# Performance work log

Measured on AMD Instinct MI355X. Metric: run time of the kernel, lower is better.

Reference implementation:

```python
import jax, jax.numpy as jnp
import numpy as np

B, S, EMBED = 8, 2048, 512
FFN = 2048
N_QUBITS = 10
DEPTH = 2


def _apply_1q(state, mats, wire):
    # state: (N,) + (2,)*n complex; mats: (N,2,2) per-token or (2,2) shared
    s = jnp.moveaxis(state, 1 + wire, 1)
    shp = s.shape
    s = s.reshape(shp[0], 2, -1)
    if mats.ndim == 3:
        s = jnp.einsum('nab,nbr->nar', mats, s)
    else:
        s = jnp.einsum('ab,nbr->nar', mats, s)
    return jnp.moveaxis(s.reshape(shp), 1, 1 + wire)


def _cnot(state, ctrl, tgt):
    # CNOT: flip target axis on the control=1 slice
    ca, ta = 1 + ctrl, 1 + tgt
    s0 = jax.lax.index_in_dim(state, 0, axis=ca, keepdims=True)
    s1 = jax.lax.index_in_dim(state, 1, axis=ca, keepdims=True)
    s1 = jnp.flip(s1, axis=ta)
    return jnp.concatenate([s0, s1], axis=ca)


def _qlayer(x_flat, theta, n_qubits=N_QUBITS, depth=DEPTH):
    # x_flat: (N, n_qubits) RX encoding angles; theta: (n_qubits,) RY params
    N = x_flat.shape[0]
    state = jnp.zeros((N,) + (2,) * n_qubits, jnp.complex64)
    state = state.at[(slice(None),) + (0,) * n_qubits].set(1.0)
    # encoder: RX(x_i) on wire i, per-token angles
    for w in range(n_qubits):
        a = x_flat[:, w] * 0.5
        c = jnp.cos(a).astype(jnp.complex64)
        s = (-1j * jnp.sin(a)).astype(jnp.complex64)
        mats = jnp.stack([jnp.stack([c, s], -1), jnp.stack([s, c], -1)], -2)  # (N,2,2)
        state = _apply_1q(state, mats, w)
    # trainable RY(theta_w) on each wire (shared across tokens)
    for w in range(n_qubits):
        a = theta[w] * 0.5
        c, s = jnp.cos(a), jnp.sin(a)
        mat = jnp.stack([jnp.stack([c, -s]), jnp.stack([s, c])]).astype(jnp.complex64)
        state = _apply_1q(state, mat, w)
    # depth rounds of ring CNOT chain
    for _ in range(depth):
        for w in range(n_qubits - 1):
            state = _cnot(state, w, w + 1)
        state = _cnot(state, n_qubits - 1, 0)
    # MeasureAll PauliZ: <Z_w> per wire
    probs = jnp.abs(state.reshape(N, -1)) ** 2  # (N, 2^n)
    bits = (jnp.arange(2 ** n_qubits)[None, :] >> (n_qubits - 1 - jnp.arange(n_qubits))[:, None]) & 1
    z = (1 - 2 * bits).astype(probs.dtype)  # (n, 2^n)
    return probs @ z.T  # (N, n)


def setup_inputs() -> dict:
    key = jax.random.key(0)
    k = jax.random.split(key, 6)
    x = jax.random.normal(k[0], (B, S, EMBED), jnp.float32)
    ry_theta = jax.random.uniform(k[1], (N_QUBITS,), jnp.float32, 0.0, 2.0 * np.pi)
    W1 = jax.random.normal(k[2], (FFN, N_QUBITS), jnp.float32) / np.sqrt(N_QUBITS)
    b1 = jax.random.normal(k[3], (FFN,), jnp.float32) * 0.01
    W2 = jax.random.normal(k[4], (EMBED, FFN), jnp.float32) / np.sqrt(FFN)
    b2 = jax.random.normal(k[5], (EMBED,), jnp.float32) * 0.01
    return {"x": x, "ry_theta": ry_theta, "W1": W1, "b1": b1, "W2": W2, "b2": b2}


def reference(x, ry_theta, W1, b1, W2, b2):
    b, s, _ = x.shape
    xf = x.reshape(b * s, -1)[:, :N_QUBITS]  # encoder only uses first n_qubits feats
    q = _qlayer(xf, ry_theta).reshape(b, s, N_QUBITS)
    # dropout is identity at eval; linear1 -> relu -> linear2
    h = jax.nn.relu(q @ W1.T + b1)
    return h @ W2.T + b2
```

## Files before the change

### kernel.cpp

```cpp
#include <hip/hip_runtime.h>
#include <hip/hip_bf16.h>


typedef __attribute__((ext_vector_type(8))) short bf16x8;
typedef __attribute__((ext_vector_type(16))) float f32x16;
typedef __attribute__((ext_vector_type(8))) unsigned short us8;
typedef unsigned int u32;

#define NTOK  16384
#define EMBED 512
#define FFN   2048
#define NQ    10
#define BM    128
#define BN    128

__device__ __forceinline__ unsigned short f2bf(float f) {
  union { float f; unsigned int u; } a; a.f = f;
  unsigned int r = a.u + 0x7FFFu + ((a.u >> 16) & 1u);
  return (unsigned short)(r >> 16);
}

__device__ __forceinline__ void gload_lds16(const void* g, void* l) {
  __builtin_amdgcn_global_load_lds(
      (const __attribute__((address_space(1))) unsigned int*)g,
      (__attribute__((address_space(3))) unsigned int*)l, 16, 0, 0);
}

__global__ __launch_bounds__(256) void k_cvt_w2(const float* __restrict__ W2,
                                                unsigned short* __restrict__ W2b) {
  int gid = blockIdx.x * 256 + threadIdx.x;
  int idx = gid * 8;
  int row = idx >> 11;
  int c   = (idx >> 3) & 255;
  int pair = c >> 4, cl = c & 15;
  int slot = cl ^ (row & 15);
  float4 v0 = *(const float4*)(W2 + idx);
  float4 v1 = *(const float4*)(W2 + idx + 4);
  us8 o;
  o[0] = f2bf(v0.x); o[1] = f2bf(v0.y); o[2] = f2bf(v0.z); o[3] = f2bf(v0.w);
  o[4] = f2bf(v1.x); o[5] = f2bf(v1.y); o[6] = f2bf(v1.z); o[7] = f2bf(v1.w);
  *(us8*)(W2b + (size_t)row * FFN + pair * 128 + slot * 8) = o;
}

__global__ __launch_bounds__(256) void k_cvt_w1f(const float* __restrict__ W1,
                                                 const float* __restrict__ b1,
                                                 unsigned short* __restrict__ W1f) {
  int gid = blockIdx.x * 256 + threadIdx.x;
  int l = gid & 63, blk = gid >> 6;
  int k = blk * 32 + (l & 31);
  int wg = (l >> 5) * 8;
  us8 o;
#pragma unroll
  for (int e = 0; e < 8; ++e) {
    int wire = wg + e;
    float v = (wire < NQ) ? W1[k * NQ + wire] : (wire == NQ ? b1[k] : 0.f);
    o[e] = f2bf(v);
  }
  *(us8*)(W1f + (size_t)gid * 8) = o;
}

__global__ __launch_bounds__(256) void k_q(const float* __restrict__ x,
                                           const float* __restrict__ theta,
                                           unsigned short* __restrict__ Qf) {
  int gid = blockIdx.x * 256 + threadIdx.x;
  int l = gid & 63, tile = gid >> 6;
  int tok = tile * 32 + (l & 31), g = l >> 5;
  const int masks[NQ] = {0x2AB,0x3FD,0x3FA,0x3F5,0x3EA,0x3D5,0x3AA,0x355,0x2AA,0x155};
  float z[NQ], qv[NQ];
#pragma unroll
  for (int w = 0; w < NQ; ++w)
    z[w] = __builtin_cosf(x[(size_t)tok * EMBED + w]) * __builtin_cosf(theta[w]);
#pragma unroll
  for (int w = 0; w < NQ; ++w) {
    float p = 1.f;
#pragma unroll
    for (int v = 0; v < NQ; ++v)
      if ((masks[w] >> v) & 1) p *= z[v];
    qv[w] = p;
  }
  us8 o = (us8)0;
  if (g == 0) {
#pragma unroll
    for (int e = 0; e < 8; ++e) o[e] = f2bf(qv[e]);
  } else {
    o[0] = f2bf(qv[8]); o[1] = f2bf(qv[9]); o[2] = f2bf(1.f);
  }
  *(us8*)(Qf + (size_t)gid * 8) = o;
}

__global__ __launch_bounds__(256, 2) void k_fused(const unsigned short* __restrict__ Qf,
                                                  const unsigned short* __restrict__ W1f,
                                                  const unsigned short* __restrict__ W2b,
                                                  const float* __restrict__ b2,
                                                  float* __restrict__ out) {
  __shared__ short Bw[2][128 * 128];

  int bid = blockIdx.x;
  int swz = (bid & 7) * 64 + (bid >> 3);
  const int m0 = (swz >> 2) * BM;
  const int n0 = (swz & 3) * BN;
  const int tid  = threadIdx.x;
  const int lane = tid & 63;
  const int wave = tid >> 6;
  const int wm = wave >> 1, wn = wave & 1;
  const int h = lane >> 5, t31 = lane & 31;

  bf16x8 qf[2];
#pragma unroll
  for (int i = 0; i < 2; ++i)
    qf[i] = *(const bf16x8*)&Qf[(((size_t)(m0 >> 5) + wm * 2 + i) * 64 + lane) * 8];

  f32x16 acc[2][2] = {};
  bf16x8 wfE[2], wfO[2];
  bf16x8 aqE[2][2][2], aqO[2][2][2];

#define WLOAD(KT, WF)                                                           \
  { _Pragma("unroll")                                                           \
    for (int b = 0; b < 2; ++b)                                                 \
      WF[b] = *(const bf16x8*)&W1f[(((size_t)(KT) * 2 + b) * 64 + lane) * 8]; }

#define STAGE(P, B)                                                             \
  { _Pragma("unroll")                                                           \
    for (int i2 = 0; i2 < 8; ++i2) {                                            \
      int ch = i2 * 256 + tid, row = ch >> 4, slot = ch & 15;                   \
      gload_lds16(&W2b[(size_t)(n0 + row) * FFN + (P) * 128 + slot * 8],        \
                  &Bw[B][ch * 8]);                                              \
    } }

#define HGEN(AQ, WF)                                                            \
  { _Pragma("unroll")                                                           \
    for (int i = 0; i < 2; ++i) {                                               \
      _Pragma("unroll")                                                         \
      for (int b = 0; b < 2; ++b) {                                             \
        f32x16 zz = {};                                                         \
        f32x16 d = __builtin_amdgcn_mfma_f32_32x32x16_bf16(WF[b], qf[i], zz, 0, 0, 0); \
        u32 dw0, dw1, dw2, dw3, dw4, dw5, dw6, dw7;                             \
        { float a0=fmaxf(d[0],0.f),a1=fmaxf(d[1],0.f);                          \
          asm("v_cvt_pk_bf16_f32 %0, %1, %2":"=v"(dw0):"v"(a0),"v"(a1)); }      \
        { float a0=fmaxf(d[2],0.f),a1=fmaxf(d[3],0.f);                          \
          asm("v_cvt_pk_bf16_f32 %0, %1, %2":"=v"(dw1):"v"(a0),"v"(a1)); }      \
        { float a0=fmaxf(d[4],0.f),a1=fmaxf(d[5],0.f);                          \
          asm("v_cvt_pk_bf16_f32 %0, %1, %2":"=v"(dw2):"v"(a0),"v"(a1)); }      \
        { float a0=fmaxf(d[6],0.f),a1=fmaxf(d[7],0.f);                          \
          asm("v_cvt_pk_bf16_f32 %0, %1, %2":"=v"(dw3):"v"(a0),"v"(a1)); }      \
        { float a0=fmaxf(d[8],0.f),a1=fmaxf(d[9],0.f);                          \
          asm("v_cvt_pk_bf16_f32 %0, %1, %2":"=v"(dw4):"v"(a0),"v"(a1)); }      \
        { float a0=fmaxf(d[10],0.f),a1=fmaxf(d[11],0.f);                        \
          asm("v_cvt_pk_bf16_f32 %0, %1, %2":"=v"(dw5):"v"(a0),"v"(a1)); }      \
        { float a0=fmaxf(d[12],0.f),a1=fmaxf(d[13],0.f);                        \
          asm("v_cvt_pk_bf16_f32 %0, %1, %2":"=v"(dw6):"v"(a0),"v"(a1)); }      \
        { float a0=fmaxf(d[14],0.f),a1=fmaxf(d[15],0.f);                        \
          asm("v_cvt_pk_bf16_f32 %0, %1, %2":"=v"(dw7):"v"(a0),"v"(a1)); }      \
        asm("v_permlane32_swap_b32 %0, %1" : "+v"(dw0), "+v"(dw2));             \
        asm("v_permlane32_swap_b32 %0, %1" : "+v"(dw1), "+v"(dw3));             \
        asm("v_permlane32_swap_b32 %0, %1" : "+v"(dw4), "+v"(dw6));             \
        asm("v_permlane32_swap_b32 %0, %1" : "+v"(dw5), "+v"(dw7));             \
        union { u32 u[4]; bf16x8 v; } u0, u1;                                   \
        u0.u[0]=dw0; u0.u[1]=dw1; u0.u[2]=dw2; u0.u[3]=dw3;                     \
        u1.u[0]=dw4; u1.u[1]=dw5; u1.u[2]=dw6; u1.u[3]=dw7;                     \
        AQ[i][b][0] = u0.v; AQ[i][b][1] = u1.v;                                 \
      } } }

#define GEMMKT(KPAR, AQ, BUF)                                                   \
  { _Pragma("unroll")                                                           \
    for (int b = 0; b < 2; ++b) {                                               \
      _Pragma("unroll")                                                         \
      for (int sb = 0; sb < 2; ++sb) {                                          \
        bf16x8 bg0, bg1;                                                        \
        { int row = wn * 64 + t31;                                              \
          int c = (KPAR) * 8 + b * 4 + sb * 2 + h;                              \
          bg0 = *(const bf16x8*)((const char*)&Bw[BUF][0] + row * 256 +         \
                                 (c ^ (row & 15)) * 16); }                      \
        { int row = wn * 64 + 32 + t31;                                         \
          int c = (KPAR) * 8 + b * 4 + sb * 2 + h;                              \
          bg1 = *(const bf16x8*)((const char*)&Bw[BUF][0] + row * 256 +         \
                                 (c ^ (row & 15)) * 16); }                      \
        __builtin_amdgcn_s_setprio(1);                                          \
        acc[0][0] = __builtin_amdgcn_mfma_f32_32x32x16_bf16(AQ[0][b][sb], bg0, acc[0][0], 0, 0, 0); \
        acc[0][1] = __builtin_amdgcn_mfma_f32_32x32x16_bf16(AQ[0][b][sb], bg1, acc[0][1], 0, 0, 0); \
        acc[1][0] = __builtin_amdgcn_mfma_f32_32x32x16_bf16(AQ[1][b][sb], bg0, acc[1][0], 0, 0, 0); \
        acc[1][1] = __builtin_amdgcn_mfma_f32_32x32x16_bf16(AQ[1][b][sb], bg1, acc[1][1], 0, 0, 0); \
        __builtin_amdgcn_s_setprio(0);                                          \
      } } }

  WLOAD(0, wfE);
  WLOAD(1, wfO);
  STAGE(0, 0);
  STAGE(1, 1);
  HGEN(aqE, wfE);

  for (int p = 0; p < 16; ++p) {
    asm volatile("s_waitcnt vmcnt(0)" ::: "memory");
    __builtin_amdgcn_s_barrier();
    if (p < 15) STAGE(p + 1, (p + 1) & 1);
    const int buf = p & 1;
    if (p < 15) WLOAD(2 * p + 2, wfE);
    GEMMKT(0, aqE, buf);
    HGEN(aqO, wfO);
    if (p < 15) {
      WLOAD(2 * p + 3, wfO);
      GEMMKT(1, aqO, buf);
      HGEN(aqE, wfE);
    } else {
      GEMMKT(1, aqO, buf);
    }
  }

#pragma unroll
  for (int j = 0; j < 2; ++j) {
    const int col = n0 + wn * 64 + j * 32 + t31;
    const float bbv = b2[col];
#pragma unroll
    for (int i = 0; i < 2; ++i) {
#pragma unroll
      for (int r = 0; r < 16; ++r) {
        int tok = m0 + wm * 64 + i * 32 + (r & 3) + 8 * (r >> 2) + 4 * h;
        out[(size_t)tok * EMBED + col] = acc[i][j][r] + bbv;
      }
    }
  }
#undef WLOAD
#undef STAGE
#undef HGEN
#undef GEMMKT
}

extern "C" void kernel_launch(void* const* d_in, const int* in_sizes, int n_in,
                              void* d_out, int out_size, void* d_ws, size_t ws_size,
                              hipStream_t stream) {
  const float* x     = (const float*)d_in[0];
  const float* theta = (const float*)d_in[1];
  const float* W1    = (const float*)d_in[2];
  const float* b1    = (const float*)d_in[3];
  const float* W2    = (const float*)d_in[4];
  const float* b2    = (const float*)d_in[5];
  float* out = (float*)d_out;

  char* ws = (char*)d_ws;
  unsigned short* W2b = (unsigned short*)ws;
  unsigned short* W1f = (unsigned short*)(ws + (2u << 20));
  unsigned short* Qfg = (unsigned short*)(ws + (2u << 20) + (64u << 10));

  k_cvt_w2 <<<(EMBED * FFN) / (256 * 8), 256, 0, stream>>>(W2, W2b);
  k_cvt_w1f<<<16, 256, 0, stream>>>(W1, b1, W1f);
  k_q      <<<128, 256, 0, stream>>>(x, theta, Qfg);
  k_fused  <<<(NTOK / BM) * (EMBED / BN), 256, 0, stream>>>(Qfg, W1f, W2b, b2, out);
}
```

Before: 63.51 us.

## Load W2 fragments directly from global into registers, dropping LDS staging

W2 is now pre-converted into an MFMA-fragment layout so each lane can load its B operand straight from global/L2 into registers. This removes the shared-memory double buffer, the global-to-LDS copies and the per-stage barrier, and adds register double-buffering (bgA/bgB) to overlap loads with the MFMAs. The trade-off is that each wave reloads W2 from the cache hierarchy, since the two wm waves in a block no longer share one LDS copy. Register pressure also rises, which may hurt occupancy at two blocks per CU.

```diff
diff --git a/kernel.cpp b/kernel.cpp
--- a/kernel.cpp
+++ b/kernel.cpp
@@ -20,26 +20,19 @@
   return (unsigned short)(r >> 16);
 }
 
-__device__ __forceinline__ void gload_lds16(const void* g, void* l) {
-  __builtin_amdgcn_global_load_lds(
-      (const __attribute__((address_space(1))) unsigned int*)g,
-      (__attribute__((address_space(3))) unsigned int*)l, 16, 0, 0);
-}
-
-__global__ __launch_bounds__(256) void k_cvt_w2(const float* __restrict__ W2,
-                                                unsigned short* __restrict__ W2b) {
+__global__ __launch_bounds__(256) void k_cvt_w2f(const float* __restrict__ W2,
+                                                 unsigned short* __restrict__ W2f) {
   int gid = blockIdx.x * 256 + threadIdx.x;
-  int idx = gid * 8;
-  int row = idx >> 11;
-  int c   = (idx >> 3) & 255;
-  int pair = c >> 4, cl = c & 15;
-  int slot = cl ^ (row & 15);
-  float4 v0 = *(const float4*)(W2 + idx);
-  float4 v1 = *(const float4*)(W2 + idx + 4);
+  int l = gid & 63, kb = (gid >> 6) & 127, tile = gid >> 13;
+  int col = tile * 32 + (l & 31);
+  int k0 = kb * 16 + (l >> 5) * 8;
+  const float* src = W2 + (size_t)col * FFN + k0;
+  float4 v0 = *(const float4*)src;
+  float4 v1 = *(const float4*)(src + 4);
   us8 o;
   o[0] = f2bf(v0.x); o[1] = f2bf(v0.y); o[2] = f2bf(v0.z); o[3] = f2bf(v0.w);
   o[4] = f2bf(v1.x); o[5] = f2bf(v1.y); o[6] = f2bf(v1.z); o[7] = f2bf(v1.w);
-  *(us8*)(W2b + (size_t)row * FFN + pair * 128 + slot * 8) = o;
+  *(us8*)(W2f + (size_t)gid * 8) = o;
 }
 
 __global__ __launch_bounds__(256) void k_cvt_w1f(const float* __restrict__ W1,
@@ -90,11 +83,9 @@
 
 __global__ __launch_bounds__(256, 2) void k_fused(const unsigned short* __restrict__ Qf,
                                                   const unsigned short* __restrict__ W1f,
-                                                  const unsigned short* __restrict__ W2b,
+                                                  const unsigned short* __restrict__ W2f,
                                                   const float* __restrict__ b2,
                                                   float* __restrict__ out) {
-  __shared__ short Bw[2][128 * 128];
-
   int bid = blockIdx.x;
   int swz = (bid & 7) * 64 + (bid >> 3);
   const int m0 = (swz >> 2) * BM;
@@ -112,19 +103,21 @@
 
   f32x16 acc[2][2] = {};
   bf16x8 wfE[2], wfO[2];
-  bf16x8 aqE[2][2][2], aqO[2][2][2];
+  bf16x8 aqA[2][2][2], aqB[2][2][2];
+  bf16x8 bgA[8], bgB[8];
 
 #define WLOAD(KT, WF)                                                           \
   { _Pragma("unroll")                                                           \
     for (int b = 0; b < 2; ++b)                                                 \
       WF[b] = *(const bf16x8*)&W1f[(((size_t)(KT) * 2 + b) * 64 + lane) * 8]; }
 
-#define STAGE(P, B)                                                             \
+#define BGLOAD(P, HF, BG)                                                       \
   { _Pragma("unroll")                                                           \
-    for (int i2 = 0; i2 < 8; ++i2) {                                            \
-      int ch = i2 * 256 + tid, row = ch >> 4, slot = ch & 15;                   \
-      gload_lds16(&W2b[(size_t)(n0 + row) * FFN + (P) * 128 + slot * 8],        \
-                  &Bw[B][ch * 8]);                                              \
+    for (int r = 0; r < 8; ++r) {                                               \
+      int j = r >> 2, s = r & 3;                                                \
+      int tile = (n0 >> 5) + wn * 2 + j;                                        \
+      int kb = (P) * 8 + (HF) * 4 + s;                                          \
+      BG[r] = *(const bf16x8*)&W2f[(((size_t)tile * 128 + kb) * 64 + lane) * 8]; \
     } }
 
 #define HGEN(AQ, WF)                                                            \
@@ -161,49 +154,30 @@
         AQ[i][b][0] = u0.v; AQ[i][b][1] = u1.v;                                 \
       } } }
 
-#define GEMMKT(KPAR, AQ, BUF)                                                   \
-  { _Pragma("unroll")                                                           \
-    for (int b = 0; b < 2; ++b) {                                               \
-      _Pragma("unroll")                                                         \
-      for (int sb = 0; sb < 2; ++sb) {                                          \
-        bf16x8 bg0, bg1;                                                        \
-        { int row = wn * 64 + t31;                                              \
-          int c = (KPAR) * 8 + b * 4 + sb * 2 + h;                              \
-          bg0 = *(const bf16x8*)((const char*)&Bw[BUF][0] + row * 256 +         \
-                                 (c ^ (row & 15)) * 16); }                      \
-        { int row = wn * 64 + 32 + t31;                                         \
-          int c = (KPAR) * 8 + b * 4 + sb * 2 + h;                              \
-          bg1 = *(const bf16x8*)((const char*)&Bw[BUF][0] + row * 256 +         \
-                                 (c ^ (row & 15)) * 16); }                      \
-        __builtin_amdgcn_s_setprio(1);                                          \
-        acc[0][0] = __builtin_amdgcn_mfma_f32_32x32x16_bf16(AQ[0][b][sb], bg0, acc[0][0], 0, 0, 0); \
-        acc[0][1] = __builtin_amdgcn_mfma_f32_32x32x16_bf16(AQ[0][b][sb], bg1, acc[0][1], 0, 0, 0); \
-        acc[1][0] = __builtin_amdgcn_mfma_f32_32x32x16_bf16(AQ[1][b][sb], bg0, acc[1][0], 0, 0, 0); \
-        acc[1][1] = __builtin_amdgcn_mfma_f32_32x32x16_bf16(AQ[1][b][sb], bg1, acc[1][1], 0, 0, 0); \
-        __builtin_amdgcn_s_setprio(0);                                          \
-      } } }
+#define GEMMKT(AQ, BG)                                                          \
+  { __builtin_amdgcn_s_setprio(1);                                              \
+    _Pragma("unroll")                                                           \
+    for (int s = 0; s < 4; ++s) {                                               \
+      acc[0][0] = __builtin_amdgcn_mfma_f32_32x32x16_bf16(AQ[0][s >> 1][s & 1], BG[s],     acc[0][0], 0, 0, 0); \
+      acc[0][1] = __builtin_amdgcn_mfma_f32_32x32x16_bf16(AQ[0][s >> 1][s & 1], BG[4 + s], acc[0][1], 0, 0, 0); \
+      acc[1][0] = __builtin_amdgcn_mfma_f32_32x32x16_bf16(AQ[1][s >> 1][s & 1], BG[s],     acc[1][0], 0, 0, 0); \
+      acc[1][1] = __builtin_amdgcn_mfma_f32_32x32x16_bf16(AQ[1][s >> 1][s & 1], BG[4 + s], acc[1][1], 0, 0, 0); \
+    }                                                                           \
+    __builtin_amdgcn_s_setprio(0); }
 
   WLOAD(0, wfE);
   WLOAD(1, wfO);
-  STAGE(0, 0);
-  STAGE(1, 1);
-  HGEN(aqE, wfE);
+  BGLOAD(0, 0, bgA);
+  HGEN(aqA, wfE);
 
   for (int p = 0; p < 16; ++p) {
-    asm volatile("s_waitcnt vmcnt(0)" ::: "memory");
-    __builtin_amdgcn_s_barrier();
-    if (p < 15) STAGE(p + 1, (p + 1) & 1);
-    const int buf = p & 1;
+    BGLOAD(p, 1, bgB);
     if (p < 15) WLOAD(2 * p + 2, wfE);
-    GEMMKT(0, aqE, buf);
-    HGEN(aqO, wfO);
-    if (p < 15) {
-      WLOAD(2 * p + 3, wfO);
-      GEMMKT(1, aqO, buf);
-      HGEN(aqE, wfE);
-    } else {
-      GEMMKT(1, aqO, buf);
-    }
+    GEMMKT(aqA, bgA);
+    HGEN(aqB, wfO);
+    if (p < 15) { BGLOAD(p + 1, 0, bgA); WLOAD(2 * p + 3, wfO); }
+    GEMMKT(aqB, bgB);
+    if (p < 15) HGEN(aqA, wfE);
   }
 
 #pragma unroll
@@ -220,7 +194,7 @@
     }
   }
 #undef WLOAD
-#undef STAGE
+#undef BGLOAD
 #undef HGEN
 #undef GEMMKT
 }
@@ -237,12 +211,12 @@
   float* out = (float*)d_out;
 
   char* ws = (char*)d_ws;
-  unsigned short* W2b = (unsigned short*)ws;
+  unsigned short* W2f = (unsigned short*)ws;
   unsigned short* W1f = (unsigned short*)(ws + (2u << 20));
   unsigned short* Qfg = (unsigned short*)(ws + (2u << 20) + (64u << 10));
 
-  k_cvt_w2 <<<(EMBED * FFN) / (256 * 8), 256, 0, stream>>>(W2, W2b);
+  k_cvt_w2f<<<512, 256, 0, stream>>>(W2, W2f);
   k_cvt_w1f<<<16, 256, 0, stream>>>(W1, b1, W1f);
   k_q      <<<128, 256, 0, stream>>>(x, theta, Qfg);
-  k_fused  <<<(NTOK / BM) * (EMBED / BN), 256, 0, stream>>>(Qfg, W1f, W2b, b2, out);
-}
+  k_fused  <<<(NTOK / BM) * (EMBED / BN), 256, 0, stream>>>(Qfg, W1f, W2f, b2, out);
+}
```

After: 65.48 us. 1.03x slower.
